# Optimization experiments

Hardware: AMD Instinct MI355X
Metric: run time of the kernel (lower is better)

The kernel has to match this reference:

```python
import jax, jax.numpy as jnp
import numpy as np

NEG_INF = np.finfo(np.float32).min


def setup_inputs() -> dict:
    key = jax.random.key(0)
    ks = jax.random.split(key, 7)
    N, K, H = 30000, 32, 128
    return {
        "h_V": jax.random.normal(ks[0], (N, H), jnp.float32),
        "h_E": jax.random.normal(ks[1], (N, K, H), jnp.float32),
        "mask_attend": jax.random.randint(ks[2], (N, K), 0, 2, jnp.int32),
        "W_Q": jax.random.normal(ks[3], (H, H), jnp.float32) * (1.0 / np.sqrt(H)),
        "W_K": jax.random.normal(ks[4], (H, H), jnp.float32) * (1.0 / np.sqrt(H)),
        "W_V": jax.random.normal(ks[5], (H, H), jnp.float32) * (1.0 / np.sqrt(H)),
        "W_O": jax.random.normal(ks[6], (H, H), jnp.float32) * (1.0 / np.sqrt(H)),
    }


def reference(h_V, h_E, mask_attend, W_Q, W_K, W_V, W_O):
    n_heads = 4
    N, K, Hd = h_E.shape
    d = Hd // n_heads
    # nn.Linear(bias=False): y = x @ W.T
    Q = (h_V @ W_Q.T).reshape(N, n_heads, d)          # [N, h, d]
    Kk = (h_E @ W_K.T).reshape(N, K, n_heads, d)      # [N, K, h, d]
    V = (h_E @ W_V.T).reshape(N, K, n_heads, d)       # [N, K, h, d]
    logits = jnp.einsum('nhd,nkhd->nhk', Q, Kk) / np.float32(np.sqrt(d))  # [N, h, K]
    mask = mask_attend.astype(logits.dtype)[:, None, :]                   # [N, 1, K]
    logits = jnp.where(mask > 0, logits, jnp.float32(NEG_INF))
    attend = jax.nn.softmax(logits, axis=-1) * mask                       # [N, h, K]
    out = jnp.einsum('nhk,nkhd->nhd', attend, V).reshape(N, Hd)
    return out @ W_O.T
```

## Files before the change

### kernel.cpp

```cpp
#include <hip/hip_runtime.h>

#define NEG_INF (-3.402823466e+38f)
#define SCALE 0.17677669529663689f

typedef __attribute__((ext_vector_type(8))) short bf16x8;
typedef __attribute__((ext_vector_type(4))) float f32x4;
typedef __attribute__((ext_vector_type(4))) unsigned short u16x4;

__device__ __forceinline__ unsigned short f2bf(float f) {
  union { float f; unsigned u; } v; v.f = f;
  unsigned r = v.u + 0x7fffu + ((v.u >> 16) & 1u);
  return (unsigned short)(r >> 16);
}

__device__ __forceinline__ bf16x8 pack_bf8(const float* __restrict__ p) {
  float4 a = *(const float4*)p;
  float4 b = *(const float4*)(p + 4);
  bf16x8 r;
  r[0] = (short)f2bf(a.x); r[1] = (short)f2bf(a.y);
  r[2] = (short)f2bf(a.z); r[3] = (short)f2bf(a.w);
  r[4] = (short)f2bf(b.x); r[5] = (short)f2bf(b.y);
  r[6] = (short)f2bf(b.z); r[7] = (short)f2bf(b.w);
  return r;
}

__global__ __launch_bounds__(256) void fuse_weights(
    const float* __restrict__ wq, const float* __restrict__ wk,
    const float* __restrict__ wv, const float* __restrict__ wo,
    unsigned short* __restrict__ MT, unsigned short* __restrict__ WB) {
  const int w = (blockIdx.x * 256 + threadIdx.x) >> 6;
  const int lane = threadIdx.x & 63;
  const int lr = lane & 15, lk = lane >> 4;
  const int h = w >> 6, t2 = w & 63, jt = t2 >> 3, it = t2 & 7;

  bf16x8 a, b;
#pragma unroll
  for (int j = 0; j < 8; ++j) {
    a[j] = (short)f2bf(wq[(h * 32 + lk * 8 + j) * 128 + jt * 16 + lr]);
    b[j] = (short)f2bf(wk[(h * 32 + lk * 8 + j) * 128 + it * 16 + lr]);
  }
  f32x4 c = (f32x4){0.f, 0.f, 0.f, 0.f};
  c = __builtin_amdgcn_mfma_f32_16x16x32_bf16(a, b, c, 0, 0, 0);
#pragma unroll
  for (int r = 0; r < 4; ++r)
    MT[h * 16384 + (it * 16 + lr) * 128 + jt * 16 + lk * 4 + r] = f2bf(c[r]);

  bf16x8 a2 = pack_bf8(wo + (jt * 16 + lr) * 128 + h * 32 + lk * 8);
  bf16x8 b2;
#pragma unroll
  for (int j = 0; j < 8; ++j)
    b2[j] = (short)f2bf(wv[(h * 32 + lk * 8 + j) * 128 + it * 16 + lr]);
  f32x4 c2 = (f32x4){0.f, 0.f, 0.f, 0.f};
  c2 = __builtin_amdgcn_mfma_f32_16x16x32_bf16(a2, b2, c2, 0, 0, 0);
#pragma unroll
  for (int r = 0; r < 4; ++r)
    WB[(size_t)(jt * 16 + lk * 4 + r) * 512 + h * 128 + it * 16 + lr] = f2bf(c2[r]);
}

__global__ __launch_bounds__(256) void gemm_wq(
    const float* __restrict__ X, const unsigned short* __restrict__ MT,
    unsigned short* __restrict__ WQb, int M) {
  __shared__ unsigned short Wl[128 * 136];
  const int wave = threadIdx.x >> 6, lane = threadIdx.x & 63;
  const int lr = lane & 15, lk = lane >> 4;
  const int row0 = blockIdx.x * 64 + wave * 16;
  const int arow = row0 + lr;

  bf16x8 af[4];
  if (arow < M) {
    const float* xr = X + (size_t)arow * 128;
#pragma unroll
    for (int kk = 0; kk < 4; ++kk) af[kk] = pack_bf8(xr + kk * 32 + lk * 8);
  } else {
#pragma unroll
    for (int kk = 0; kk < 4; ++kk) af[kk] = (bf16x8)(short)0;
  }

  for (int h = 0; h < 4; ++h) {
    __syncthreads();
    const unsigned short* Wsrc = MT + (size_t)h * 16384;
    for (int idx = threadIdx.x; idx < 2048; idx += 256) {
      int row = idx >> 4, col = (idx & 15) * 8;
      *(bf16x8*)&Wl[row * 136 + col] = *(const bf16x8*)(Wsrc + row * 128 + col);
    }
    __syncthreads();

    f32x4 acc[8];
#pragma unroll
    for (int ct = 0; ct < 8; ++ct) acc[ct] = (f32x4){0.f, 0.f, 0.f, 0.f};
#pragma unroll
    for (int kk = 0; kk < 4; ++kk)
#pragma unroll
      for (int ct = 0; ct < 8; ++ct) {
        bf16x8 b = *(const bf16x8*)&Wl[(ct * 16 + lr) * 136 + kk * 32 + lk * 8];
        acc[ct] = __builtin_amdgcn_mfma_f32_16x16x32_bf16(af[kk], b, acc[ct], 0, 0, 0);
      }

#pragma unroll
    for (int ct = 0; ct < 8; ++ct)
#pragma unroll
      for (int r = 0; r < 4; ++r) {
        int row = row0 + lk * 4 + r;
        if (row < M)
          WQb[(size_t)row * 512 + h * 128 + ct * 16 + lr] = f2bf(acc[ct][r]);
      }
  }
}

__global__ __launch_bounds__(256, 4) void neigh_aE(
    const float* __restrict__ hE, const int* __restrict__ mask,
    const unsigned short* __restrict__ WQb, unsigned short* __restrict__ aEb,
    int N) {
  __shared__ unsigned short Elds[4][32 * 136];
  __shared__ unsigned short attL[4][128];

  const int wave = threadIdx.x >> 6, lane = threadIdx.x & 63;
  const int lr = lane & 15, lk = lane >> 4;
  unsigned short* El = Elds[wave];
  unsigned short* at = attL[wave];
  const int n = blockIdx.x * 4 + wave;
  if (n >= N) return;

  const float* E = hE + (size_t)n * 4096;
  float4 raw[16];
#pragma unroll
  for (int q = 0; q < 8; ++q) {
    const float* p = E + ((q >> 2) * 16 + lr) * 128 + (q & 3) * 32 + lk * 8;
    raw[q * 2] = *(const float4*)p;
    raw[q * 2 + 1] = *(const float4*)(p + 4);
  }
  bf16x8 bq[4];
#pragma unroll
  for (int kk = 0; kk < 4; ++kk)
    bq[kk] = *(const bf16x8*)(WQb + (size_t)n * 512 + (lr & 3) * 128 + kk * 32 + lk * 8);
  const int4 m0 = *(const int4*)(mask + (size_t)n * 32 + lk * 4);
  const int4 m1 = *(const int4*)(mask + (size_t)n * 32 + 16 + lk * 4);

  bf16x8 af[2][4];
#pragma unroll
  for (int q = 0; q < 8; ++q) {
    float4 a = raw[q * 2], b = raw[q * 2 + 1];
    bf16x8 t;
    t[0] = (short)f2bf(a.x); t[1] = (short)f2bf(a.y);
    t[2] = (short)f2bf(a.z); t[3] = (short)f2bf(a.w);
    t[4] = (short)f2bf(b.x); t[5] = (short)f2bf(b.y);
    t[6] = (short)f2bf(b.z); t[7] = (short)f2bf(b.w);
    af[q >> 2][q & 3] = t;
    *(bf16x8*)&El[((q >> 2) * 16 + lr) * 136 + (q & 3) * 32 + lk * 8] = t;
  }

  f32x4 c0 = (f32x4){0.f, 0.f, 0.f, 0.f};
  f32x4 c1 = (f32x4){0.f, 0.f, 0.f, 0.f};
#pragma unroll
  for (int kk = 0; kk < 4; ++kk) {
    c0 = __builtin_amdgcn_mfma_f32_16x16x32_bf16(af[0][kk], bq[kk], c0, 0, 0, 0);
    c1 = __builtin_amdgcn_mfma_f32_16x16x32_bf16(af[1][kk], bq[kk], c1, 0, 0, 0);
  }

  float l[2][4];
  l[0][0] = m0.x ? c0[0] * SCALE : NEG_INF;
  l[0][1] = m0.y ? c0[1] * SCALE : NEG_INF;
  l[0][2] = m0.z ? c0[2] * SCALE : NEG_INF;
  l[0][3] = m0.w ? c0[3] * SCALE : NEG_INF;
  l[1][0] = m1.x ? c1[0] * SCALE : NEG_INF;
  l[1][1] = m1.y ? c1[1] * SCALE : NEG_INF;
  l[1][2] = m1.z ? c1[2] * SCALE : NEG_INF;
  l[1][3] = m1.w ? c1[3] * SCALE : NEG_INF;

  float mx = l[0][0];
#pragma unroll
  for (int rt = 0; rt < 2; ++rt)
#pragma unroll
    for (int r = 0; r < 4; ++r) mx = fmaxf(mx, l[rt][r]);
  mx = fmaxf(mx, __shfl_xor(mx, 16, 64));
  mx = fmaxf(mx, __shfl_xor(mx, 32, 64));

  float e[2][4];
  float sum = 0.f;
#pragma unroll
  for (int rt = 0; rt < 2; ++rt)
#pragma unroll
    for (int r = 0; r < 4; ++r) { e[rt][r] = __expf(l[rt][r] - mx); sum += e[rt][r]; }
  sum += __shfl_xor(sum, 16, 64);
  sum += __shfl_xor(sum, 32, 64);
  const float inv = 1.0f / sum;

  if (lr < 4) {
    u16x4 p0, p1;
    p0[0] = f2bf(m0.x ? e[0][0] * inv : 0.f);
    p0[1] = f2bf(m0.y ? e[0][1] * inv : 0.f);
    p0[2] = f2bf(m0.z ? e[0][2] * inv : 0.f);
    p0[3] = f2bf(m0.w ? e[0][3] * inv : 0.f);
    p1[0] = f2bf(m1.x ? e[1][0] * inv : 0.f);
    p1[1] = f2bf(m1.y ? e[1][1] * inv : 0.f);
    p1[2] = f2bf(m1.z ? e[1][2] * inv : 0.f);
    p1[3] = f2bf(m1.w ? e[1][3] * inv : 0.f);
    *(u16x4*)&at[lr * 32 + lk * 4] = p0;
    *(u16x4*)&at[lr * 32 + 16 + lk * 4] = p1;
  }

  bf16x8 attA = *(const bf16x8*)&at[(lr & 3) * 32 + lk * 8];
#pragma unroll
  for (int ct = 0; ct < 8; ++ct) {
    bf16x8 bE;
#pragma unroll
    for (int j = 0; j < 8; ++j)
      bE[j] = (short)El[(lk * 8 + j) * 136 + ct * 16 + lr];
    f32x4 acc = (f32x4){0.f, 0.f, 0.f, 0.f};
    acc = __builtin_amdgcn_mfma_f32_16x16x32_bf16(attA, bE, acc, 0, 0, 0);
    float v = (lk == 0) ? acc[0] : (lk == 1) ? acc[1] : (lk == 2) ? acc[2] : acc[3];
    aEb[(size_t)n * 512 + lk * 128 + ct * 16 + lr] = f2bf(v);
  }
}

__global__ __launch_bounds__(256) void gemm_out(
    const unsigned short* __restrict__ aEb, const unsigned short* __restrict__ WB,
    float* __restrict__ Y, int M) {
  __shared__ unsigned short Wl[128 * 136];
  const int wave = threadIdx.x >> 6, lane = threadIdx.x & 63;
  const int lr = lane & 15, lk = lane >> 4;
  const int row0 = blockIdx.x * 64 + wave * 16;
  const int arow = row0 + lr;

  f32x4 acc[8];
#pragma unroll
  for (int ct = 0; ct < 8; ++ct) acc[ct] = (f32x4){0.f, 0.f, 0.f, 0.f};

  for (int h = 0; h < 4; ++h) {
    __syncthreads();
    for (int idx = threadIdx.x; idx < 2048; idx += 256) {
      int row = idx >> 4, col = (idx & 15) * 8;
      *(bf16x8*)&Wl[row * 136 + col] = *(const bf16x8*)(WB + (size_t)row * 512 + h * 128 + col);
    }
    __syncthreads();

    bf16x8 af[4];
    if (arow < M) {
#pragma unroll
      for (int kk = 0; kk < 4; ++kk)
        af[kk] = *(const bf16x8*)(aEb + (size_t)arow * 512 + h * 128 + kk * 32 + lk * 8);
    } else {
#pragma unroll
      for (int kk = 0; kk < 4; ++kk) af[kk] = (bf16x8)(short)0;
    }
#pragma unroll
    for (int kk = 0; kk < 4; ++kk)
#pragma unroll
      for (int ct = 0; ct < 8; ++ct) {
        bf16x8 b = *(const bf16x8*)&Wl[(ct * 16 + lr) * 136 + kk * 32 + lk * 8];
        acc[ct] = __builtin_amdgcn_mfma_f32_16x16x32_bf16(af[kk], b, acc[ct], 0, 0, 0);
      }
  }

#pragma unroll
  for (int ct = 0; ct < 8; ++ct)
#pragma unroll
    for (int r = 0; r < 4; ++r) {
      int row = row0 + lk * 4 + r;
      if (row < M) Y[(size_t)row * 128 + ct * 16 + lr] = acc[ct][r];
    }
}

extern "C" void kernel_launch(void* const* d_in, const int* in_sizes, int n_in,
                              void* d_out, int out_size, void* d_ws, size_t ws_size,
                              hipStream_t stream) {
  const float* hV = (const float*)d_in[0];
  const float* hE = (const float*)d_in[1];
  const int* mask = (const int*)d_in[2];
  const float* Wq = (const float*)d_in[3];
  const float* Wk = (const float*)d_in[4];
  const float* Wv = (const float*)d_in[5];
  const float* Wo = (const float*)d_in[6];
  float* out = (float*)d_out;
  const int N = in_sizes[0] / 128;

  char* ws = (char*)d_ws;
  unsigned short* MT = (unsigned short*)(ws);
  unsigned short* WB = (unsigned short*)(ws + 131072);
  unsigned short* WQb = (unsigned short*)(ws + 262144);
  unsigned short* aEb = (unsigned short*)(ws + 262144 + (size_t)N * 1024);

  fuse_weights<<<64, 256, 0, stream>>>(Wq, Wk, Wv, Wo, MT, WB);
  gemm_wq<<<(N + 63) / 64, 256, 0, stream>>>(hV, MT, WQb, N);
  neigh_aE<<<(N + 3) / 4, 256, 0, stream>>>(hE, mask, WQb, aEb, N);
  gemm_out<<<(N + 63) / 64, 256, 0, stream>>>(aEb, WB, out, N);
}
```

Before: 149.8 us.

## Fuse query projection, neighbor attention and output projection into one kernel

```diff
diff --git a/kernel.cpp b/kernel.cpp
--- a/kernel.cpp
+++ b/kernel.cpp
@@ -6,6 +6,8 @@
 typedef __attribute__((ext_vector_type(8))) short bf16x8;
 typedef __attribute__((ext_vector_type(4))) float f32x4;
 typedef __attribute__((ext_vector_type(4))) unsigned short u16x4;
+
+#define WA_PITCH 536
 
 __device__ __forceinline__ unsigned short f2bf(float f) {
   union { float f; unsigned u; } v; v.f = f;
@@ -57,208 +59,175 @@
     WB[(size_t)(jt * 16 + lk * 4 + r) * 512 + h * 128 + it * 16 + lr] = f2bf(c2[r]);
 }
 
-__global__ __launch_bounds__(256) void gemm_wq(
-    const float* __restrict__ X, const unsigned short* __restrict__ MT,
-    unsigned short* __restrict__ WQb, int M) {
-  __shared__ unsigned short Wl[128 * 136];
+__global__ __launch_bounds__(256, 3) void neigh_fused(
+    const float* __restrict__ hV, const float* __restrict__ hE,
+    const int* __restrict__ mask, const unsigned short* __restrict__ MT,
+    const unsigned short* __restrict__ WB, float* __restrict__ out, int N) {
+  __shared__ unsigned short Elds[4][32 * 136];
+  __shared__ unsigned short WA[16 * WA_PITCH];
+  __shared__ unsigned short attL[4][128];
+
   const int wave = threadIdx.x >> 6, lane = threadIdx.x & 63;
   const int lr = lane & 15, lk = lane >> 4;
-  const int row0 = blockIdx.x * 64 + wave * 16;
-  const int arow = row0 + lr;
-
-  bf16x8 af[4];
-  if (arow < M) {
-    const float* xr = X + (size_t)arow * 128;
-#pragma unroll
-    for (int kk = 0; kk < 4; ++kk) af[kk] = pack_bf8(xr + kk * 32 + lk * 8);
-  } else {
-#pragma unroll
-    for (int kk = 0; kk < 4; ++kk) af[kk] = (bf16x8)(short)0;
-  }
-
-  for (int h = 0; h < 4; ++h) {
-    __syncthreads();
-    const unsigned short* Wsrc = MT + (size_t)h * 16384;
-    for (int idx = threadIdx.x; idx < 2048; idx += 256) {
-      int row = idx >> 4, col = (idx & 15) * 8;
-      *(bf16x8*)&Wl[row * 136 + col] = *(const bf16x8*)(Wsrc + row * 128 + col);
-    }
-    __syncthreads();
-
-    f32x4 acc[8];
-#pragma unroll
-    for (int ct = 0; ct < 8; ++ct) acc[ct] = (f32x4){0.f, 0.f, 0.f, 0.f};
+  const int n0 = blockIdx.x * 16;
+
+  float* hVl = (float*)&Elds[0][0];
+  {
+    const int row = threadIdx.x >> 4, c0 = (threadIdx.x & 15) * 8;
+    const int gn = min(n0 + row, N - 1);
+    const float* src = hV + (size_t)gn * 128 + c0;
+    *(float4*)&hVl[row * 128 + c0] = *(const float4*)src;
+    *(float4*)&hVl[row * 128 + c0 + 4] = *(const float4*)(src + 4);
+  }
+  __syncthreads();
+
+  {
+    bf16x8 a1[4];
 #pragma unroll
     for (int kk = 0; kk < 4; ++kk)
+      a1[kk] = pack_bf8(hVl + lr * 128 + kk * 32 + lk * 8);
+
+    const unsigned short* MTh = MT + wave * 16384;
+    f32x4 p1[8];
+#pragma unroll
+    for (int ct = 0; ct < 8; ++ct) p1[ct] = (f32x4){0.f, 0.f, 0.f, 0.f};
+#pragma unroll
+    for (int kk = 0; kk < 4; ++kk)
 #pragma unroll
       for (int ct = 0; ct < 8; ++ct) {
-        bf16x8 b = *(const bf16x8*)&Wl[(ct * 16 + lr) * 136 + kk * 32 + lk * 8];
-        acc[ct] = __builtin_amdgcn_mfma_f32_16x16x32_bf16(af[kk], b, acc[ct], 0, 0, 0);
+        bf16x8 b = *(const bf16x8*)(MTh + (ct * 16 + lr) * 128 + kk * 32 + lk * 8);
+        p1[ct] = __builtin_amdgcn_mfma_f32_16x16x32_bf16(a1[kk], b, p1[ct], 0, 0, 0);
       }
-
 #pragma unroll
     for (int ct = 0; ct < 8; ++ct)
 #pragma unroll
-      for (int r = 0; r < 4; ++r) {
-        int row = row0 + lk * 4 + r;
-        if (row < M)
-          WQb[(size_t)row * 512 + h * 128 + ct * 16 + lr] = f2bf(acc[ct][r]);
-      }
-  }
-}
-
-__global__ __launch_bounds__(256, 4) void neigh_aE(
-    const float* __restrict__ hE, const int* __restrict__ mask,
-    const unsigned short* __restrict__ WQb, unsigned short* __restrict__ aEb,
-    int N) {
-  __shared__ unsigned short Elds[4][32 * 136];
-  __shared__ unsigned short attL[4][128];
-
-  const int wave = threadIdx.x >> 6, lane = threadIdx.x & 63;
-  const int lr = lane & 15, lk = lane >> 4;
+      for (int r = 0; r < 4; ++r)
+        WA[(lk * 4 + r) * WA_PITCH + wave * 128 + ct * 16 + lr] = f2bf(p1[ct][r]);
+  }
+  __syncthreads();
+
   unsigned short* El = Elds[wave];
   unsigned short* at = attL[wave];
-  const int n = blockIdx.x * 4 + wave;
-  if (n >= N) return;
-
-  const float* E = hE + (size_t)n * 4096;
-  float4 raw[16];
-#pragma unroll
-  for (int q = 0; q < 8; ++q) {
-    const float* p = E + ((q >> 2) * 16 + lr) * 128 + (q & 3) * 32 + lk * 8;
-    raw[q * 2] = *(const float4*)p;
-    raw[q * 2 + 1] = *(const float4*)(p + 4);
-  }
-  bf16x8 bq[4];
-#pragma unroll
-  for (int kk = 0; kk < 4; ++kk)
-    bq[kk] = *(const bf16x8*)(WQb + (size_t)n * 512 + (lr & 3) * 128 + kk * 32 + lk * 8);
-  const int4 m0 = *(const int4*)(mask + (size_t)n * 32 + lk * 4);
-  const int4 m1 = *(const int4*)(mask + (size_t)n * 32 + 16 + lk * 4);
-
-  bf16x8 af[2][4];
-#pragma unroll
-  for (int q = 0; q < 8; ++q) {
-    float4 a = raw[q * 2], b = raw[q * 2 + 1];
-    bf16x8 t;
-    t[0] = (short)f2bf(a.x); t[1] = (short)f2bf(a.y);
-    t[2] = (short)f2bf(a.z); t[3] = (short)f2bf(a.w);
-    t[4] = (short)f2bf(b.x); t[5] = (short)f2bf(b.y);
-    t[6] = (short)f2bf(b.z); t[7] = (short)f2bf(b.w);
-    af[q >> 2][q & 3] = t;
-    *(bf16x8*)&El[((q >> 2) * 16 + lr) * 136 + (q & 3) * 32 + lk * 8] = t;
-  }
-
-  f32x4 c0 = (f32x4){0.f, 0.f, 0.f, 0.f};
-  f32x4 c1 = (f32x4){0.f, 0.f, 0.f, 0.f};
-#pragma unroll
-  for (int kk = 0; kk < 4; ++kk) {
-    c0 = __builtin_amdgcn_mfma_f32_16x16x32_bf16(af[0][kk], bq[kk], c0, 0, 0, 0);
-    c1 = __builtin_amdgcn_mfma_f32_16x16x32_bf16(af[1][kk], bq[kk], c1, 0, 0, 0);
-  }
-
-  float l[2][4];
-  l[0][0] = m0.x ? c0[0] * SCALE : NEG_INF;
-  l[0][1] = m0.y ? c0[1] * SCALE : NEG_INF;
-  l[0][2] = m0.z ? c0[2] * SCALE : NEG_INF;
-  l[0][3] = m0.w ? c0[3] * SCALE : NEG_INF;
-  l[1][0] = m1.x ? c1[0] * SCALE : NEG_INF;
-  l[1][1] = m1.y ? c1[1] * SCALE : NEG_INF;
-  l[1][2] = m1.z ? c1[2] * SCALE : NEG_INF;
-  l[1][3] = m1.w ? c1[3] * SCALE : NEG_INF;
-
-  float mx = l[0][0];
-#pragma unroll
-  for (int rt = 0; rt < 2; ++rt)
-#pragma unroll
-    for (int r = 0; r < 4; ++r) mx = fmaxf(mx, l[rt][r]);
-  mx = fmaxf(mx, __shfl_xor(mx, 16, 64));
-  mx = fmaxf(mx, __shfl_xor(mx, 32, 64));
-
-  float e[2][4];
-  float sum = 0.f;
-#pragma unroll
-  for (int rt = 0; rt < 2; ++rt)
-#pragma unroll
-    for (int r = 0; r < 4; ++r) { e[rt][r] = __expf(l[rt][r] - mx); sum += e[rt][r]; }
-  sum += __shfl_xor(sum, 16, 64);
-  sum += __shfl_xor(sum, 32, 64);
-  const float inv = 1.0f / sum;
-
-  if (lr < 4) {
-    u16x4 p0, p1;
-    p0[0] = f2bf(m0.x ? e[0][0] * inv : 0.f);
-    p0[1] = f2bf(m0.y ? e[0][1] * inv : 0.f);
-    p0[2] = f2bf(m0.z ? e[0][2] * inv : 0.f);
-    p0[3] = f2bf(m0.w ? e[0][3] * inv : 0.f);
-    p1[0] = f2bf(m1.x ? e[1][0] * inv : 0.f);
-    p1[1] = f2bf(m1.y ? e[1][1] * inv : 0.f);
-    p1[2] = f2bf(m1.z ? e[1][2] * inv : 0.f);
-    p1[3] = f2bf(m1.w ? e[1][3] * inv : 0.f);
-    *(u16x4*)&at[lr * 32 + lk * 4] = p0;
-    *(u16x4*)&at[lr * 32 + 16 + lk * 4] = p1;
-  }
-
-  bf16x8 attA = *(const bf16x8*)&at[(lr & 3) * 32 + lk * 8];
-#pragma unroll
-  for (int ct = 0; ct < 8; ++ct) {
-    bf16x8 bE;
-#pragma unroll
-    for (int j = 0; j < 8; ++j)
-      bE[j] = (short)El[(lk * 8 + j) * 136 + ct * 16 + lr];
-    f32x4 acc = (f32x4){0.f, 0.f, 0.f, 0.f};
-    acc = __builtin_amdgcn_mfma_f32_16x16x32_bf16(attA, bE, acc, 0, 0, 0);
-    float v = (lk == 0) ? acc[0] : (lk == 1) ? acc[1] : (lk == 2) ? acc[2] : acc[3];
-    aEb[(size_t)n * 512 + lk * 128 + ct * 16 + lr] = f2bf(v);
-  }
-}
-
-__global__ __launch_bounds__(256) void gemm_out(
-    const unsigned short* __restrict__ aEb, const unsigned short* __restrict__ WB,
-    float* __restrict__ Y, int M) {
-  __shared__ unsigned short Wl[128 * 136];
-  const int wave = threadIdx.x >> 6, lane = threadIdx.x & 63;
-  const int lr = lane & 15, lk = lane >> 4;
-  const int row0 = blockIdx.x * 64 + wave * 16;
-  const int arow = row0 + lr;
-
-  f32x4 acc[8];
-#pragma unroll
-  for (int ct = 0; ct < 8; ++ct) acc[ct] = (f32x4){0.f, 0.f, 0.f, 0.f};
-
-  for (int h = 0; h < 4; ++h) {
-    __syncthreads();
-    for (int idx = threadIdx.x; idx < 2048; idx += 256) {
-      int row = idx >> 4, col = (idx & 15) * 8;
-      *(bf16x8*)&Wl[row * 136 + col] = *(const bf16x8*)(WB + (size_t)row * 512 + h * 128 + col);
-    }
-    __syncthreads();
-
-    bf16x8 af[4];
-    if (arow < M) {
-#pragma unroll
-      for (int kk = 0; kk < 4; ++kk)
-        af[kk] = *(const bf16x8*)(aEb + (size_t)arow * 512 + h * 128 + kk * 32 + lk * 8);
-    } else {
-#pragma unroll
-      for (int kk = 0; kk < 4; ++kk) af[kk] = (bf16x8)(short)0;
-    }
+#pragma unroll 1
+  for (int it = 0; it < 4; ++it) {
+    const int m = wave * 4 + it;
+    const int n = min(n0 + m, N - 1);
+
+    const float* E = hE + (size_t)n * 4096;
+    float4 raw[16];
+#pragma unroll
+    for (int q = 0; q < 8; ++q) {
+      const float* p = E + ((q >> 2) * 16 + lr) * 128 + (q & 3) * 32 + lk * 8;
+      raw[q * 2] = *(const float4*)p;
+      raw[q * 2 + 1] = *(const float4*)(p + 4);
+    }
+    bf16x8 bq[4];
 #pragma unroll
     for (int kk = 0; kk < 4; ++kk)
-#pragma unroll
-      for (int ct = 0; ct < 8; ++ct) {
-        bf16x8 b = *(const bf16x8*)&Wl[(ct * 16 + lr) * 136 + kk * 32 + lk * 8];
-        acc[ct] = __builtin_amdgcn_mfma_f32_16x16x32_bf16(af[kk], b, acc[ct], 0, 0, 0);
+      bq[kk] = *(const bf16x8*)&WA[m * WA_PITCH + (lr & 3) * 128 + kk * 32 + lk * 8];
+    const int4 m0 = *(const int4*)(mask + (size_t)n * 32 + lk * 4);
+    const int4 m1 = *(const int4*)(mask + (size_t)n * 32 + 16 + lk * 4);
+
+    bf16x8 af[2][4];
+#pragma unroll
+    for (int q = 0; q < 8; ++q) {
+      float4 a = raw[q * 2], b = raw[q * 2 + 1];
+      bf16x8 t;
+      t[0] = (short)f2bf(a.x); t[1] = (short)f2bf(a.y);
+      t[2] = (short)f2bf(a.z); t[3] = (short)f2bf(a.w);
+      t[4] = (short)f2bf(b.x); t[5] = (short)f2bf(b.y);
+      t[6] = (short)f2bf(b.z); t[7] = (short)f2bf(b.w);
+      af[q >> 2][q & 3] = t;
+      *(bf16x8*)&El[((q >> 2) * 16 + lr) * 136 + (q & 3) * 32 + lk * 8] = t;
+    }
+
+    f32x4 c0 = (f32x4){0.f, 0.f, 0.f, 0.f};
+    f32x4 c1 = (f32x4){0.f, 0.f, 0.f, 0.f};
+#pragma unroll
+    for (int kk = 0; kk < 4; ++kk) {
+      c0 = __builtin_amdgcn_mfma_f32_16x16x32_bf16(af[0][kk], bq[kk], c0, 0, 0, 0);
+      c1 = __builtin_amdgcn_mfma_f32_16x16x32_bf16(af[1][kk], bq[kk], c1, 0, 0, 0);
+    }
+
+    float l[2][4];
+    l[0][0] = m0.x ? c0[0] * SCALE : NEG_INF;
+    l[0][1] = m0.y ? c0[1] * SCALE : NEG_INF;
+    l[0][2] = m0.z ? c0[2] * SCALE : NEG_INF;
+    l[0][3] = m0.w ? c0[3] * SCALE : NEG_INF;
+    l[1][0] = m1.x ? c1[0] * SCALE : NEG_INF;
+    l[1][1] = m1.y ? c1[1] * SCALE : NEG_INF;
+    l[1][2] = m1.z ? c1[2] * SCALE : NEG_INF;
+    l[1][3] = m1.w ? c1[3] * SCALE : NEG_INF;
+
+    float mx = l[0][0];
+#pragma unroll
+    for (int rt = 0; rt < 2; ++rt)
+#pragma unroll
+      for (int r = 0; r < 4; ++r) mx = fmaxf(mx, l[rt][r]);
+    mx = fmaxf(mx, __shfl_xor(mx, 16, 64));
+    mx = fmaxf(mx, __shfl_xor(mx, 32, 64));
+
+    float e[2][4];
+    float sum = 0.f;
+#pragma unroll
+    for (int rt = 0; rt < 2; ++rt)
+#pragma unroll
+      for (int r = 0; r < 4; ++r) { e[rt][r] = __expf(l[rt][r] - mx); sum += e[rt][r]; }
+    sum += __shfl_xor(sum, 16, 64);
+    sum += __shfl_xor(sum, 32, 64);
+    const float inv = 1.0f / sum;
+
+    if (lr < 4) {
+      u16x4 p0, p1;
+      p0[0] = f2bf(m0.x ? e[0][0] * inv : 0.f);
+      p0[1] = f2bf(m0.y ? e[0][1] * inv : 0.f);
+      p0[2] = f2bf(m0.z ? e[0][2] * inv : 0.f);
+      p0[3] = f2bf(m0.w ? e[0][3] * inv : 0.f);
+      p1[0] = f2bf(m1.x ? e[1][0] * inv : 0.f);
+      p1[1] = f2bf(m1.y ? e[1][1] * inv : 0.f);
+      p1[2] = f2bf(m1.z ? e[1][2] * inv : 0.f);
+      p1[3] = f2bf(m1.w ? e[1][3] * inv : 0.f);
+      *(u16x4*)&at[lr * 32 + lk * 4] = p0;
+      *(u16x4*)&at[lr * 32 + 16 + lk * 4] = p1;
+    }
+
+    bf16x8 attA = *(const bf16x8*)&at[(lr & 3) * 32 + lk * 8];
+#pragma unroll
+    for (int ct = 0; ct < 8; ++ct) {
+      bf16x8 bE;
+#pragma unroll
+      for (int j = 0; j < 8; ++j)
+        bE[j] = (short)El[(lk * 8 + j) * 136 + ct * 16 + lr];
+      f32x4 acc = (f32x4){0.f, 0.f, 0.f, 0.f};
+      acc = __builtin_amdgcn_mfma_f32_16x16x32_bf16(attA, bE, acc, 0, 0, 0);
+      float v = (lk == 0) ? acc[0] : (lk == 1) ? acc[1] : (lk == 2) ? acc[2] : acc[3];
+      WA[m * WA_PITCH + lk * 128 + ct * 16 + lr] = f2bf(v);
+    }
+  }
+  __syncthreads();
+
+  {
+    f32x4 po[2];
+    po[0] = (f32x4){0.f, 0.f, 0.f, 0.f};
+    po[1] = (f32x4){0.f, 0.f, 0.f, 0.f};
+#pragma unroll
+    for (int kk = 0; kk < 16; ++kk) {
+      bf16x8 aA = *(const bf16x8*)&WA[lr * WA_PITCH + kk * 32 + lk * 8];
+#pragma unroll
+      for (int c = 0; c < 2; ++c) {
+        const int ct = wave * 2 + c;
+        bf16x8 b = *(const bf16x8*)(WB + (size_t)(ct * 16 + lr) * 512 + kk * 32 + lk * 8);
+        po[c] = __builtin_amdgcn_mfma_f32_16x16x32_bf16(aA, b, po[c], 0, 0, 0);
       }
-  }
-
-#pragma unroll
-  for (int ct = 0; ct < 8; ++ct)
-#pragma unroll
-    for (int r = 0; r < 4; ++r) {
-      int row = row0 + lk * 4 + r;
-      if (row < M) Y[(size_t)row * 128 + ct * 16 + lr] = acc[ct][r];
-    }
+    }
+#pragma unroll
+    for (int c = 0; c < 2; ++c)
+#pragma unroll
+      for (int r = 0; r < 4; ++r) {
+        const int row = n0 + lk * 4 + r;
+        if (row < N) out[(size_t)row * 128 + (wave * 2 + c) * 16 + lr] = po[c][r];
+      }
+  }
 }
 
 extern "C" void kernel_launch(void* const* d_in, const int* in_sizes, int n_in,
@@ -277,11 +246,7 @@
   char* ws = (char*)d_ws;
   unsigned short* MT = (unsigned short*)(ws);
   unsigned short* WB = (unsigned short*)(ws + 131072);
-  unsigned short* WQb = (unsigned short*)(ws + 262144);
-  unsigned short* aEb = (unsigned short*)(ws + 262144 + (size_t)N * 1024);
 
   fuse_weights<<<64, 256, 0, stream>>>(Wq, Wk, Wv, Wo, MT, WB);
-  gemm_wq<<<(N + 63) / 64, 256, 0, stream>>>(hV, MT, WQb, N);
-  neigh_aE<<<(N + 3) / 4, 256, 0, stream>>>(hE, mask, WQb, aEb, N);
-  gemm_out<<<(N + 63) / 64, 256, 0, stream>>>(aEb, WB, out, N);
-}
+  neigh_fused<<<(N + 15) / 16, 256, 0, stream>>>(hV, hE, mask, MT, WB, out, N);
+}
```

After: 153.1 us. +2.2%, slower.
